# Optimization experiments

Measured on AMD Instinct MI355X. Metric: run time of the kernel, lower is better.

## Reference

```python
import jax, jax.numpy as jnp
import numpy as np

MARGIN = 1.0
EPS = 1e-16


def _pairwise_dist(x):
    # Euclidean cdist, p=2: sqrt(||a||^2 + ||b||^2 - 2 a.b), clamped, with
    # a safe sqrt so the (zero-distance) diagonal has zero gradient like torch.cdist.
    sq = jnp.sum(x * x, axis=1)  # [N]
    d2 = sq[:, None] + sq[None, :] - 2.0 * (x @ x.T)  # [N, N]
    d2 = jnp.maximum(d2, 0.0)
    return jnp.where(d2 > 0.0, jnp.sqrt(jnp.where(d2 > 0.0, d2, 1.0)), 0.0)


def setup_inputs() -> dict:
    key = jax.random.key(0)
    k1, k2 = jax.random.split(key)
    embeddings = jax.random.normal(k1, (384, 512), dtype=jnp.float32)
    labels = jax.random.randint(k2, (384,), 0, 24, dtype=jnp.int64)
    return {"embeddings": embeddings, "labels": labels}


def reference(embeddings, labels):
    dist = _pairwise_dist(embeddings)  # [N, N]
    pos = (labels[:, None] == labels[None, :]).astype(embeddings.dtype)  # [N, N]
    neg = 1.0 - pos
    positive_dist = dist * pos
    negative_dist = dist * neg
    # triplet_loss[a, p, n] = d(a,p)*pos - d(a,n)*neg + margin
    triplet_loss = jax.nn.relu(positive_dist[:, :, None] - negative_dist[:, None, :] + MARGIN)
    valid = pos[:, :, None] * neg[:, None, :]  # [N, N, N]
    num_valid = jnp.sum(valid) + EPS
    return jnp.sum(triplet_loss * valid) / num_valid
```

## Files before the change

kernel.cpp:

```cpp
#include <hip/hip_runtime.h>


#define NPTS 384
#define DIM  512
#define TS   32
#define BK   64
#define PITCH 68
#define NT1  256
#define NT2  384

__global__ __launch_bounds__(NT1) void dist_tile(const float* __restrict__ X,
                                                 float* __restrict__ D) {
    __shared__ float As[TS * PITCH];
    __shared__ float Bs[TS * PITCH];
    const int t  = threadIdx.x;
    const int tx = t & 15, ty = t >> 4;
    const int bi = blockIdx.y * TS;
    const int bj = blockIdx.x * TS;

    const float4* X4 = (const float4*)X;
    const int r0 = t >> 4, c4 = t & 15;

    float4 pa0, pa1, pb0, pb1;
    int k4 = 0;
    {
        pa0 = X4[(size_t)(bi + r0)      * (DIM/4) + k4 + c4];
        pa1 = X4[(size_t)(bi + r0 + 16) * (DIM/4) + k4 + c4];
        pb0 = X4[(size_t)(bj + r0)      * (DIM/4) + k4 + c4];
        pb1 = X4[(size_t)(bj + r0 + 16) * (DIM/4) + k4 + c4];
        *(float4*)&As[ r0       * PITCH + c4*4] = pa0;
        *(float4*)&As[(r0 + 16) * PITCH + c4*4] = pa1;
        *(float4*)&Bs[ r0       * PITCH + c4*4] = pb0;
        *(float4*)&Bs[(r0 + 16) * PITCH + c4*4] = pb1;
    }
    __syncthreads();

    float acc00 = 0.f, acc01 = 0.f, acc10 = 0.f, acc11 = 0.f;

    for (int kt = 0; kt < DIM / BK; ++kt) {
        if (kt < DIM / BK - 1) {
            k4 = (kt + 1) * (BK / 4);
            pa0 = X4[(size_t)(bi + r0)      * (DIM/4) + k4 + c4];
            pa1 = X4[(size_t)(bi + r0 + 16) * (DIM/4) + k4 + c4];
            pb0 = X4[(size_t)(bj + r0)      * (DIM/4) + k4 + c4];
            pb1 = X4[(size_t)(bj + r0 + 16) * (DIM/4) + k4 + c4];
        }
#pragma unroll
        for (int kk = 0; kk < BK / 4; ++kk) {
            const float4 a0 = *(const float4*)&As[(2*ty)   * PITCH + kk*4];
            const float4 a1 = *(const float4*)&As[(2*ty+1) * PITCH + kk*4];
            const float4 b0 = *(const float4*)&Bs[(2*tx)   * PITCH + kk*4];
            const float4 b1 = *(const float4*)&Bs[(2*tx+1) * PITCH + kk*4];
            float d;
            d = a0.x - b0.x; acc00 = fmaf(d, d, acc00);
            d = a0.y - b0.y; acc00 = fmaf(d, d, acc00);
            d = a0.z - b0.z; acc00 = fmaf(d, d, acc00);
            d = a0.w - b0.w; acc00 = fmaf(d, d, acc00);
            d = a0.x - b1.x; acc01 = fmaf(d, d, acc01);
            d = a0.y - b1.y; acc01 = fmaf(d, d, acc01);
            d = a0.z - b1.z; acc01 = fmaf(d, d, acc01);
            d = a0.w - b1.w; acc01 = fmaf(d, d, acc01);
            d = a1.x - b0.x; acc10 = fmaf(d, d, acc10);
            d = a1.y - b0.y; acc10 = fmaf(d, d, acc10);
            d = a1.z - b0.z; acc10 = fmaf(d, d, acc10);
            d = a1.w - b0.w; acc10 = fmaf(d, d, acc10);
            d = a1.x - b1.x; acc11 = fmaf(d, d, acc11);
            d = a1.y - b1.y; acc11 = fmaf(d, d, acc11);
            d = a1.z - b1.z; acc11 = fmaf(d, d, acc11);
            d = a1.w - b1.w; acc11 = fmaf(d, d, acc11);
        }
        __syncthreads();
        if (kt < DIM / BK - 1) {
            *(float4*)&As[ r0       * PITCH + c4*4] = pa0;
            *(float4*)&As[(r0 + 16) * PITCH + c4*4] = pa1;
            *(float4*)&Bs[ r0       * PITCH + c4*4] = pb0;
            *(float4*)&Bs[(r0 + 16) * PITCH + c4*4] = pb1;
            __syncthreads();
        }
    }

    const int gi = bi + 2*ty, gj = bj + 2*tx;
    *(float2*)&D[(size_t)gi      * NPTS + gj] = make_float2(sqrtf(acc00), sqrtf(acc01));
    *(float2*)&D[(size_t)(gi+1)  * NPTS + gj] = make_float2(sqrtf(acc10), sqrtf(acc11));
}

__global__ __launch_bounds__(NT2) void pair_sums(const float* __restrict__ D,
                                                 const int* __restrict__ labels,
                                                 float* __restrict__ psum,
                                                 unsigned* __restrict__ pcnt) {
    __shared__ float s_dp[NPTS];
    __shared__ float s_dn[NPTS];
    __shared__ int   s_cp[NT2 / 64], s_cn[NT2 / 64];
    __shared__ float s_wred[NT2 / 64];

    const int t = threadIdx.x, lane = t & 63, w = t >> 6;
    const int a = blockIdx.x;
    const int lab_a = labels[a];

    const float dv  = D[(size_t)a * NPTS + t];
    const bool  isp = (labels[t] == lab_a);

    const unsigned long long m = __ballot(isp);
    if (lane == 0) { s_cp[w] = __popcll(m); s_cn[w] = 64 - __popcll(m); }
    __syncthreads();

    int basep = 0, basen = 0, np = 0, nn = 0;
#pragma unroll
    for (int i = 0; i < NT2 / 64; ++i) {
        if (i < w) { basep += s_cp[i]; basen += s_cn[i]; }
        np += s_cp[i]; nn += s_cn[i];
    }
    const unsigned long long blw = (1ull << lane) - 1ull;
    if (isp) s_dp[basep + __popcll(m  & blw)] = dv;
    else     s_dn[basen + __popcll(~m & blw)] = dv;
    __syncthreads();

    float local = 0.f;
    for (int p = 0; p < np; ++p) {
        const float c = s_dp[p] + 1.0f;
        for (int n = t; n < nn; n += NT2) {
            const float v = c - s_dn[n];
            local += (v > 0.f) ? v : 0.f;
        }
    }
    for (int off = 32; off; off >>= 1) local += __shfl_down(local, off, 64);
    if (lane == 0) s_wred[w] = local;
    __syncthreads();
    if (t == 0) {
        float bs = 0.f;
        for (int i = 0; i < NT2 / 64; ++i) bs += s_wred[i];
        psum[a] = bs;
        pcnt[a] = (unsigned)(np * nn);
    }
}

__global__ __launch_bounds__(NT2) void reduce_final(
    const float* __restrict__ psum, const unsigned* __restrict__ pcnt,
    float* __restrict__ out)
{
    __shared__ float s_s[NT2 / 64];
    __shared__ unsigned long long s_c[NT2 / 64];
    const int t = threadIdx.x;
    float s = psum[t];
    unsigned long long c = (unsigned long long)pcnt[t];
    for (int off = 32; off; off >>= 1) {
        s += __shfl_down(s, off, 64);
        c += __shfl_down(c, off, 64);
    }
    if ((t & 63) == 0) { s_s[t >> 6] = s; s_c[t >> 6] = c; }
    __syncthreads();
    if (t == 0) {
        float ts = 0.f; unsigned long long tc = 0ull;
        for (int w = 0; w < NT2 / 64; ++w) { ts += s_s[w]; tc += s_c[w]; }
        *out = (float)((double)ts / ((double)tc + 1e-16));
    }
}

extern "C" void kernel_launch(void* const* d_in, const int* in_sizes, int n_in,
                              void* d_out, int out_size, void* d_ws, size_t ws_size,
                              hipStream_t stream) {
    (void)in_sizes; (void)n_in; (void)out_size; (void)ws_size;
    const float* X = (const float*)d_in[0];
    const int* labels = (const int*)d_in[1];

    float*    Dmat = (float*)d_ws;
    float*    psum = (float*)((char*)d_ws + (size_t)NPTS * NPTS * 4);
    unsigned* pcnt = (unsigned*)((char*)d_ws + (size_t)NPTS * NPTS * 4 + NPTS * 4);

    dist_tile  <<<dim3(NPTS / TS, NPTS / TS), dim3(NT1), 0, stream>>>(X, Dmat);
    pair_sums  <<<dim3(NPTS),                 dim3(NT2), 0, stream>>>(Dmat, labels, psum, pcnt);
    reduce_final<<<dim3(1),                   dim3(NT2), 0, stream>>>(psum, pcnt, (float*)d_out);
}
```

Measured before the change: 75.39 us.

## Split-K distance tiles and fuse final reduction via atomic ticket

The distance kernel now uses 32x16 tiles with 128 threads and splits the K dimension in two, writing partial squared distances to two buffers, so it launches far more blocks to fill the GPU. The pair kernel sums the two partials and takes the sqrt. It then accumulates the global sum and count with atomics and a last-block ticket, which removes the separate final reduce kernel launch. The cost is an extra D-sized buffer to write and read, plus non-deterministic float atomic summation order.

```diff
diff --git a/kernel.cpp b/kernel.cpp
--- a/kernel.cpp
+++ b/kernel.cpp
@@ -3,54 +3,73 @@
 
 #define NPTS 384
 #define DIM  512
-#define TS   32
+#define TSI  32
+#define TSJ  16
 #define BK   64
 #define PITCH 68
-#define NT1  256
+#define NT1  128
 #define NT2  384
+#define KSPLIT 2
 
-__global__ __launch_bounds__(NT1) void dist_tile(const float* __restrict__ X,
-                                                 float* __restrict__ D) {
-    __shared__ float As[TS * PITCH];
-    __shared__ float Bs[TS * PITCH];
+__global__ __launch_bounds__(NT1) void dist_tile(
+    const float* __restrict__ X,
+    float* __restrict__ D0, float* __restrict__ D1,
+    float* __restrict__ ws_sum, unsigned long long* __restrict__ ws_cnt,
+    unsigned* __restrict__ ws_ticket)
+{
+    __shared__ float As[TSI * PITCH];
+    __shared__ float Bs[TSJ * PITCH];
     const int t  = threadIdx.x;
-    const int tx = t & 15, ty = t >> 4;
-    const int bi = blockIdx.y * TS;
-    const int bj = blockIdx.x * TS;
+    const int tx = t & 7, ty = t >> 3;
+    const int bj = blockIdx.x * TSJ;
+    const int bi = blockIdx.y * TSI;
+    const int kz = blockIdx.z;
+
+    if (blockIdx.x == 0 && blockIdx.y == 0 && kz == 0 && t == 0) {
+        *ws_sum = 0.0f; *ws_cnt = 0ull; *ws_ticket = 0u;
+    }
 
     const float4* X4 = (const float4*)X;
-    const int r0 = t >> 4, c4 = t & 15;
+    const int r = t >> 4, c4 = t & 15;
+    const int kb4 = kz * (DIM / KSPLIT / 4);
 
-    float4 pa0, pa1, pb0, pb1;
-    int k4 = 0;
+    float4 pa0, pa1, pa2, pa3, pb0, pb1;
     {
-        pa0 = X4[(size_t)(bi + r0)      * (DIM/4) + k4 + c4];
-        pa1 = X4[(size_t)(bi + r0 + 16) * (DIM/4) + k4 + c4];
-        pb0 = X4[(size_t)(bj + r0)      * (DIM/4) + k4 + c4];
-        pb1 = X4[(size_t)(bj + r0 + 16) * (DIM/4) + k4 + c4];
-        *(float4*)&As[ r0       * PITCH + c4*4] = pa0;
-        *(float4*)&As[(r0 + 16) * PITCH + c4*4] = pa1;
-        *(float4*)&Bs[ r0       * PITCH + c4*4] = pb0;
-        *(float4*)&Bs[(r0 + 16) * PITCH + c4*4] = pb1;
+        const int k4 = kb4 + c4;
+        pa0 = X4[(size_t)(bi + r)      * 128 + k4];
+        pa1 = X4[(size_t)(bi + r + 8)  * 128 + k4];
+        pa2 = X4[(size_t)(bi + r + 16) * 128 + k4];
+        pa3 = X4[(size_t)(bi + r + 24) * 128 + k4];
+        pb0 = X4[(size_t)(bj + r)      * 128 + k4];
+        pb1 = X4[(size_t)(bj + r + 8)  * 128 + k4];
+        *(float4*)&As[(r)      * PITCH + c4 * 4] = pa0;
+        *(float4*)&As[(r + 8)  * PITCH + c4 * 4] = pa1;
+        *(float4*)&As[(r + 16) * PITCH + c4 * 4] = pa2;
+        *(float4*)&As[(r + 24) * PITCH + c4 * 4] = pa3;
+        *(float4*)&Bs[(r)      * PITCH + c4 * 4] = pb0;
+        *(float4*)&Bs[(r + 8)  * PITCH + c4 * 4] = pb1;
     }
     __syncthreads();
 
     float acc00 = 0.f, acc01 = 0.f, acc10 = 0.f, acc11 = 0.f;
+    const int NKT = DIM / KSPLIT / BK;
 
-    for (int kt = 0; kt < DIM / BK; ++kt) {
-        if (kt < DIM / BK - 1) {
-            k4 = (kt + 1) * (BK / 4);
-            pa0 = X4[(size_t)(bi + r0)      * (DIM/4) + k4 + c4];
-            pa1 = X4[(size_t)(bi + r0 + 16) * (DIM/4) + k4 + c4];
-            pb0 = X4[(size_t)(bj + r0)      * (DIM/4) + k4 + c4];
-            pb1 = X4[(size_t)(bj + r0 + 16) * (DIM/4) + k4 + c4];
+    for (int kt = 0; kt < NKT; ++kt) {
+        if (kt < NKT - 1) {
+            const int k4 = kb4 + (kt + 1) * (BK / 4) + c4;
+            pa0 = X4[(size_t)(bi + r)      * 128 + k4];
+            pa1 = X4[(size_t)(bi + r + 8)  * 128 + k4];
+            pa2 = X4[(size_t)(bi + r + 16) * 128 + k4];
+            pa3 = X4[(size_t)(bi + r + 24) * 128 + k4];
+            pb0 = X4[(size_t)(bj + r)      * 128 + k4];
+            pb1 = X4[(size_t)(bj + r + 8)  * 128 + k4];
         }
 #pragma unroll
         for (int kk = 0; kk < BK / 4; ++kk) {
-            const float4 a0 = *(const float4*)&As[(2*ty)   * PITCH + kk*4];
-            const float4 a1 = *(const float4*)&As[(2*ty+1) * PITCH + kk*4];
-            const float4 b0 = *(const float4*)&Bs[(2*tx)   * PITCH + kk*4];
-            const float4 b1 = *(const float4*)&Bs[(2*tx+1) * PITCH + kk*4];
+            const float4 a0 = *(const float4*)&As[(2 * ty)     * PITCH + kk * 4];
+            const float4 a1 = *(const float4*)&As[(2 * ty + 1) * PITCH + kk * 4];
+            const float4 b0 = *(const float4*)&Bs[(2 * tx)     * PITCH + kk * 4];
+            const float4 b1 = *(const float4*)&Bs[(2 * tx + 1) * PITCH + kk * 4];
             float d;
             d = a0.x - b0.x; acc00 = fmaf(d, d, acc00);
             d = a0.y - b0.y; acc00 = fmaf(d, d, acc00);
@@ -70,24 +89,29 @@
             d = a1.w - b1.w; acc11 = fmaf(d, d, acc11);
         }
         __syncthreads();
-        if (kt < DIM / BK - 1) {
-            *(float4*)&As[ r0       * PITCH + c4*4] = pa0;
-            *(float4*)&As[(r0 + 16) * PITCH + c4*4] = pa1;
-            *(float4*)&Bs[ r0       * PITCH + c4*4] = pb0;
-            *(float4*)&Bs[(r0 + 16) * PITCH + c4*4] = pb1;
+        if (kt < NKT - 1) {
+            *(float4*)&As[(r)      * PITCH + c4 * 4] = pa0;
+            *(float4*)&As[(r + 8)  * PITCH + c4 * 4] = pa1;
+            *(float4*)&As[(r + 16) * PITCH + c4 * 4] = pa2;
+            *(float4*)&As[(r + 24) * PITCH + c4 * 4] = pa3;
+            *(float4*)&Bs[(r)      * PITCH + c4 * 4] = pb0;
+            *(float4*)&Bs[(r + 8)  * PITCH + c4 * 4] = pb1;
             __syncthreads();
         }
     }
 
-    const int gi = bi + 2*ty, gj = bj + 2*tx;
-    *(float2*)&D[(size_t)gi      * NPTS + gj] = make_float2(sqrtf(acc00), sqrtf(acc01));
-    *(float2*)&D[(size_t)(gi+1)  * NPTS + gj] = make_float2(sqrtf(acc10), sqrtf(acc11));
+    float* __restrict__ Dout = kz ? D1 : D0;
+    const int gi = bi + 2 * ty, gj = bj + 2 * tx;
+    *(float2*)&Dout[(size_t)gi       * NPTS + gj] = make_float2(acc00, acc01);
+    *(float2*)&Dout[(size_t)(gi + 1) * NPTS + gj] = make_float2(acc10, acc11);
 }
 
-__global__ __launch_bounds__(NT2) void pair_sums(const float* __restrict__ D,
-                                                 const int* __restrict__ labels,
-                                                 float* __restrict__ psum,
-                                                 unsigned* __restrict__ pcnt) {
+__global__ __launch_bounds__(NT2) void pair_final(
+    const float* __restrict__ D0, const float* __restrict__ D1,
+    const int* __restrict__ labels,
+    float* __restrict__ ws_sum, unsigned long long* __restrict__ ws_cnt,
+    unsigned* __restrict__ ws_ticket, float* __restrict__ out)
+{
     __shared__ float s_dp[NPTS];
     __shared__ float s_dn[NPTS];
     __shared__ int   s_cp[NT2 / 64], s_cn[NT2 / 64];
@@ -97,7 +121,7 @@
     const int a = blockIdx.x;
     const int lab_a = labels[a];
 
-    const float dv  = D[(size_t)a * NPTS + t];
+    const float dv  = sqrtf(D0[(size_t)a * NPTS + t] + D1[(size_t)a * NPTS + t]);
     const bool  isp = (labels[t] == lab_a);
 
     const unsigned long long m = __ballot(isp);
@@ -126,33 +150,19 @@
     for (int off = 32; off; off >>= 1) local += __shfl_down(local, off, 64);
     if (lane == 0) s_wred[w] = local;
     __syncthreads();
+
     if (t == 0) {
         float bs = 0.f;
         for (int i = 0; i < NT2 / 64; ++i) bs += s_wred[i];
-        psum[a] = bs;
-        pcnt[a] = (unsigned)(np * nn);
-    }
-}
-
-__global__ __launch_bounds__(NT2) void reduce_final(
-    const float* __restrict__ psum, const unsigned* __restrict__ pcnt,
-    float* __restrict__ out)
-{
-    __shared__ float s_s[NT2 / 64];
-    __shared__ unsigned long long s_c[NT2 / 64];
-    const int t = threadIdx.x;
-    float s = psum[t];
-    unsigned long long c = (unsigned long long)pcnt[t];
-    for (int off = 32; off; off >>= 1) {
-        s += __shfl_down(s, off, 64);
-        c += __shfl_down(c, off, 64);
-    }
-    if ((t & 63) == 0) { s_s[t >> 6] = s; s_c[t >> 6] = c; }
-    __syncthreads();
-    if (t == 0) {
-        float ts = 0.f; unsigned long long tc = 0ull;
-        for (int w = 0; w < NT2 / 64; ++w) { ts += s_s[w]; tc += s_c[w]; }
-        *out = (float)((double)ts / ((double)tc + 1e-16));
+        atomicAdd(ws_sum, bs);
+        atomicAdd(ws_cnt, (unsigned long long)(np * nn));
+        __threadfence();
+        const unsigned tk = atomicAdd(ws_ticket, 1u);
+        if (tk == (unsigned)gridDim.x - 1u) {
+            const float ts = atomicAdd(ws_sum, 0.0f);
+            const unsigned long long tc = atomicAdd(ws_cnt, 0ull);
+            *out = (float)((double)ts / ((double)tc + 1e-16));
+        }
     }
 }
 
@@ -163,11 +173,15 @@
     const float* X = (const float*)d_in[0];
     const int* labels = (const int*)d_in[1];
 
-    float*    Dmat = (float*)d_ws;
-    float*    psum = (float*)((char*)d_ws + (size_t)NPTS * NPTS * 4);
-    unsigned* pcnt = (unsigned*)((char*)d_ws + (size_t)NPTS * NPTS * 4 + NPTS * 4);
+    const size_t dsz = (size_t)NPTS * NPTS * sizeof(float);
+    float* D0 = (float*)d_ws;
+    float* D1 = (float*)((char*)d_ws + dsz);
+    float* ws_sum = (float*)((char*)d_ws + 2 * dsz);
+    unsigned long long* ws_cnt = (unsigned long long*)((char*)d_ws + 2 * dsz + 8);
+    unsigned* ws_ticket = (unsigned*)((char*)d_ws + 2 * dsz + 16);
 
-    dist_tile  <<<dim3(NPTS / TS, NPTS / TS), dim3(NT1), 0, stream>>>(X, Dmat);
-    pair_sums  <<<dim3(NPTS),                 dim3(NT2), 0, stream>>>(Dmat, labels, psum, pcnt);
-    reduce_final<<<dim3(1),                   dim3(NT2), 0, stream>>>(psum, pcnt, (float*)d_out);
+    dist_tile <<<dim3(NPTS / TSJ, NPTS / TSI, KSPLIT), dim3(NT1), 0, stream>>>(
+        X, D0, D1, ws_sum, ws_cnt, ws_ticket);
+    pair_final<<<dim3(NPTS), dim3(NT2), 0, stream>>>(
+        D0, D1, labels, ws_sum, ws_cnt, ws_ticket, (float*)d_out);
 }
```

New measurement: 87.59 us. 16.2% more time.
